# Kernel tuning notes

Hardware: AMD Instinct MI355X
Metric: run time of the kernel (lower is better)

The kernel has to match this reference:

```python
import jax, jax.numpy as jnp
import numpy as np

L, H, LATENT, DM, DH, FF = 4, 4, 256, 768, 192, 1024
EPS = 1e-6      # fast_transformers RecurrentLinearAttention eps
LN_EPS = 1e-5


def make_pe(d_model=LATENT, max_len=5000):
    pos = np.arange(max_len, dtype=np.float32)[:, None]
    div = np.exp(np.arange(0, d_model, 2, dtype=np.float32) * (-np.log(10000.0) / d_model))
    pe = np.zeros((max_len, d_model), np.float32)
    pe[:, 0::2] = np.sin(pos * div)
    pe[:, 1::2] = np.cos(pos * div)
    return jnp.asarray(pe)

PE = make_pe()


def layer_norm(x, g, b):
    m = x.mean(-1, keepdims=True)
    v = ((x - m) ** 2).mean(-1, keepdims=True)
    return (x - m) * jax.lax.rsqrt(v + LN_EPS) * g + b


def setup_inputs() -> dict:
    key = jax.random.key(0)
    ks = jax.random.split(key, 16)
    bs, nj, nf, T, A, C = 8, 25, 6, 80, 6, 12
    s = 0.02
    return dict(
        x=jax.random.normal(ks[0], (bs, nj, nf, T), jnp.float32),
        y=jax.random.randint(ks[1], (bs, A), 0, C),
        ind_map=jnp.sort(jax.random.randint(ks[2], (T, bs), 0, A), axis=0),
        act_tstamps=jnp.sort(jax.random.randint(ks[3], (bs, A), 1, T + 1), axis=1).at[:, -1].set(T),
        skel_W=jax.random.normal(ks[4], (nj * nf, LATENT), jnp.float32) * s,
        skel_b=jnp.zeros((LATENT,), jnp.float32),
        muQuery=jax.random.normal(ks[5], (C, LATENT), jnp.float32),
        sigmaQuery=jax.random.normal(ks[6], (C, LATENT), jnp.float32),
        Wq=jax.random.normal(ks[7], (L, DM, DM), jnp.float32) * s,
        bq=jnp.zeros((L, DM), jnp.float32),
        Wk=jax.random.normal(ks[8], (L, DM, DM), jnp.float32) * s,
        bk=jnp.zeros((L, DM), jnp.float32),
        Wv=jax.random.normal(ks[9], (L, DM, DM), jnp.float32) * s,
        bv=jnp.zeros((L, DM), jnp.float32),
        Wo=jax.random.normal(ks[10], (L, DM, DM), jnp.float32) * s,
        bo=jnp.zeros((L, DM), jnp.float32),
        W1=jax.random.normal(ks[11], (L, DM, FF), jnp.float32) * s,
        b1=jnp.zeros((L, FF), jnp.float32),
        W2=jax.random.normal(ks[12], (L, FF, DM), jnp.float32) * s,
        b2=jnp.zeros((L, DM), jnp.float32),
        ln1_g=jnp.ones((L, DM), jnp.float32), ln1_b=jnp.zeros((L, DM), jnp.float32),
        ln2_g=jnp.ones((L, DM), jnp.float32), ln2_b=jnp.zeros((L, DM), jnp.float32),
        lnf_g=jnp.ones((DM,), jnp.float32), lnf_b=jnp.zeros((DM,), jnp.float32),
    )


def _fwd(x, y, ind_map, act_tstamps, skel_W, skel_b, muQuery, sigmaQuery,
         Wq, bq, Wk, bk, Wv, bv, Wo, bo, W1, b1, W2, b2,
         ln1_g, ln1_b, ln2_g, ln2_b, lnf_g, lnf_b):
    bs, nj, nf, T = x.shape
    # skeleton embedding: [T, bs, njoints*nfeats] @ W -> [T, bs, LATENT]
    xe = x.transpose(3, 0, 1, 2).reshape(T, bs, nj * nf) @ skel_W + skel_b
    mu_q = muQuery[y]        # [bs, A, LATENT]
    sig_q = sigmaQuery[y]
    barange = jnp.arange(bs)

    @jax.checkpoint
    def step(carry, inputs):
        S, Z = carry                         # [L,bs,H,DH,DH], [L,bs,H,DH]
        t, xt, ind_t = inputs
        cm = mu_q[barange, ind_t]            # gather per-sample current action query
        cs = sig_q[barange, ind_t]
        xseq = jnp.stack([cm, cs, xt], 0)    # [3, bs, LATENT]
        start = jnp.where(t == 0, 0, t + 2)  # PositionalEncoding(last_pos=t, offset=2)
        pe3 = jax.lax.dynamic_slice_in_dim(PE, start, 3, 0)
        xseq = xseq + pe3[:, None, :]
        h = xseq.transpose(1, 0, 2).reshape(bs, 3 * LATENT)  # flatten -> [bs, DM]
        nS, nZ = [], []
        for l in range(L):
            q = (h @ Wq[l] + bq[l]).reshape(bs, H, DH)
            k = (h @ Wk[l] + bk[l]).reshape(bs, H, DH)
            v = (h @ Wv[l] + bv[l]).reshape(bs, H, DH)
            Q = jax.nn.elu(q) + 1.0          # linear-attention feature map
            K = jax.nn.elu(k) + 1.0
            Sl = S[l] + K[..., :, None] * v[..., None, :]   # state update S += k (x) v
            Zl = Z[l] + K
            inv = 1.0 / (jnp.einsum('bhd,bhd->bh', Q, Zl) + EPS)
            att = jnp.einsum('bhd,bhdm,bh->bhm', Q, Sl, inv).reshape(bs, DM)
            h1 = layer_norm(h + att @ Wo[l] + bo[l], ln1_g[l], ln1_b[l])
            ffn = jax.nn.relu(h1 @ W1[l] + b1[l]) @ W2[l] + b2[l]
            h = layer_norm(h1 + ffn, ln2_g[l], ln2_b[l])
            nS.append(Sl); nZ.append(Zl)
        h = layer_norm(h, lnf_g, lnf_b)      # encoder final norm
        return (jnp.stack(nS), jnp.stack(nZ)), h

    S0 = jnp.zeros((L, bs, H, DH, DH), x.dtype)
    Z0 = jnp.zeros((L, bs, H, DH), x.dtype)
    _, finals = jax.lax.scan(step, (S0, Z0), (jnp.arange(T), xe, ind_map))  # finals: [T,bs,DM]
    tsel = jnp.maximum(act_tstamps - 1, 0)                       # [bs, A]
    mu = finals[:, :, :LATENT][tsel, barange[:, None]]           # [bs, A, LATENT]
    logvar = finals[:, :, LATENT:2 * LATENT][tsel, barange[:, None]]
    return mu, logvar


def reference(x, y, ind_map, act_tstamps, skel_W, skel_b, muQuery, sigmaQuery,
              Wq, bq, Wk, bk, Wv, bv, Wo, bo, W1, b1, W2, b2,
              ln1_g, ln1_b, ln2_g, ln2_b, lnf_g, lnf_b):
    return _fwd(x, y, ind_map, act_tstamps, skel_W, skel_b, muQuery, sigmaQuery,
                Wq, bq, Wk, bk, Wv, bv, Wo, bo, W1, b1, W2, b2,
                ln1_g, ln1_b, ln2_g, ln2_b, lnf_g, lnf_b)
```

## Files before the change

kernel.cpp:

```cpp
#include <hip/hip_runtime.h>
#include <math.h>

#define TT 80
#define BS 8
#define NA 6
#define DMODEL 768
#define NH 4
#define DH 192
#define FFD 1024
#define NROWS (TT*BS)
#define NQKV (3*DMODEL)

typedef __bf16 bf16;
typedef __bf16 bf16x8 __attribute__((ext_vector_type(8)));
typedef float  f32x4  __attribute__((ext_vector_type(4)));

__device__ __forceinline__ float block_reduce_sum256(float v, float* sm4) {
#pragma unroll
    for (int off = 32; off > 0; off >>= 1) v += __shfl_down(v, off, 64);
    int lane = threadIdx.x & 63, wid = threadIdx.x >> 6;
    if (lane == 0) sm4[wid] = v;
    __syncthreads();
    float r = sm4[0] + sm4[1] + sm4[2] + sm4[3];
    __syncthreads();
    return r;
}

__global__ __launch_bounds__(256) void embed_k(
        const float* __restrict__ x, const int* __restrict__ y,
        const int* __restrict__ ind_map, const float* __restrict__ skel_W,
        const float* __restrict__ skel_b, const float* __restrict__ muQ,
        const float* __restrict__ sigQ, float* __restrict__ h0,
        bf16* __restrict__ h0b) {
    __shared__ float xrow[152];
    int r = blockIdx.x;
    int t = r >> 3, b = r & 7;
    int c = threadIdx.x;
    if (c < 150) xrow[c] = x[(b * 150 + c) * TT + t];
    __syncthreads();
    float acc = skel_b[c];
    for (int jf = 0; jf < 150; jf++) acc += xrow[jf] * skel_W[jf * 256 + c];
    int ind_t = ind_map[t * 8 + b];
    int yb = y[b * NA + ind_t];
    float cm = muQ[yb * 256 + c];
    float cs = sigQ[yb * 256 + c];
    int start = (t == 0) ? 0 : (t + 2);
    float div = expf((float)(c & ~1) * (-9.210340371976184f / 256.0f));
    float p0, p1, p2;
    if (c & 1) {
        p0 = cosf((float)start * div);
        p1 = cosf((float)(start + 1) * div);
        p2 = cosf((float)(start + 2) * div);
    } else {
        p0 = sinf((float)start * div);
        p1 = sinf((float)(start + 1) * div);
        p2 = sinf((float)(start + 2) * div);
    }
    float* hr = h0 + (size_t)r * DMODEL;
    float v0 = cm + p0, v1 = cs + p1, v2 = acc + p2;
    hr[c] = v0; hr[c + 256] = v1; hr[c + 512] = v2;
    bf16* hb = h0b + (size_t)r * DMODEL;
    hb[c] = (bf16)v0; hb[c + 256] = (bf16)v1; hb[c + 512] = (bf16)v2;
}

__global__ __launch_bounds__(256) void transpose_k(
        const float* __restrict__ Wq, const float* __restrict__ Wk,
        const float* __restrict__ Wv, const float* __restrict__ Wo,
        const float* __restrict__ W1, const float* __restrict__ W2,
        bf16* __restrict__ qkvT, bf16* __restrict__ woT,
        bf16* __restrict__ w1T, bf16* __restrict__ w2T) {
    int lz = blockIdx.z;
    int l = lz >> 2, z = lz & 3;
    int K = (z == 3) ? 1024 : 768;
    int N = (z == 0) ? 2304 : (z == 2) ? 1024 : 768;
    int k0 = blockIdx.x * 32, n0 = blockIdx.y * 32;
    if (k0 >= K || n0 >= N) return;
    const float* src; bf16* dst; int ldsrc; int ncol;
    if (z == 0) {
        if (n0 < 768)       { src = Wq + (size_t)l * 768 * 768; ncol = n0; }
        else if (n0 < 1536) { src = Wk + (size_t)l * 768 * 768; ncol = n0 - 768; }
        else                { src = Wv + (size_t)l * 768 * 768; ncol = n0 - 1536; }
        dst = qkvT + (size_t)l * NQKV * DMODEL; ldsrc = 768;
    } else if (z == 1) { src = Wo + (size_t)l * 768 * 768;  dst = woT + (size_t)l * 768 * 768;  ldsrc = 768;  ncol = n0; }
    else if (z == 2)   { src = W1 + (size_t)l * 768 * 1024; dst = w1T + (size_t)l * 1024 * 768; ldsrc = 1024; ncol = n0; }
    else               { src = W2 + (size_t)l * 1024 * 768; dst = w2T + (size_t)l * 768 * 1024; ldsrc = 768;  ncol = n0; }
    __shared__ float tile[32][33];
    int tx = threadIdx.x & 31, ty = threadIdx.x >> 5;
#pragma unroll
    for (int i = 0; i < 4; i++) {
        int r = ty + 8 * i;
        tile[r][tx] = src[(size_t)(k0 + r) * ldsrc + ncol + tx];
    }
    __syncthreads();
#pragma unroll
    for (int i = 0; i < 4; i++) {
        int r = ty + 8 * i;
        dst[(size_t)(n0 + r) * K + k0 + tx] = (bf16)tile[tx][r];
    }
}

template <int EPI>
__global__ __launch_bounds__(256) void gemm_mfma(
        const bf16* __restrict__ A, const bf16* __restrict__ Bt,
        const float* __restrict__ bias_q, const float* __restrict__ bias_k,
        const float* __restrict__ bias_v, const float* __restrict__ resid,
        float* __restrict__ outF, bf16* __restrict__ outB,
        int M, int N, int K) {
    __shared__ __attribute__((aligned(16))) bf16 As0[64][40];
    __shared__ __attribute__((aligned(16))) bf16 As1[64][40];
    __shared__ __attribute__((aligned(16))) bf16 Bs0[64][40];
    __shared__ __attribute__((aligned(16))) bf16 Bs1[64][40];
    int tid = threadIdx.x;
    int m0 = blockIdx.y * 64, n0 = blockIdx.x * 64;
    int w = tid >> 6;
    int l = tid & 63;
    int lm = l & 15, lq = l >> 4;
    int sr = tid >> 2;
    int sk = (tid & 3) * 8;
    const bf16* Arow = &A[(size_t)(m0 + sr) * K];
    const bf16* Brow = &Bt[(size_t)(n0 + sr) * K];
    f32x4 acc[4] = {};
    uint4 a0 = *(const uint4*)&Arow[sk];
    uint4 a1 = *(const uint4*)&Arow[32 + sk];
    uint4 b0 = *(const uint4*)&Brow[sk];
    uint4 b1 = *(const uint4*)&Brow[32 + sk];
    for (int k0 = 0; k0 < K; k0 += 64) {
        __syncthreads();
        *(uint4*)&As0[sr][sk] = a0;
        *(uint4*)&As1[sr][sk] = a1;
        *(uint4*)&Bs0[sr][sk] = b0;
        *(uint4*)&Bs1[sr][sk] = b1;
        __syncthreads();
        int k2 = k0 + 64; if (k2 >= K) k2 = 0;
        a0 = *(const uint4*)&Arow[k2 + sk];
        a1 = *(const uint4*)&Arow[k2 + 32 + sk];
        b0 = *(const uint4*)&Brow[k2 + sk];
        b1 = *(const uint4*)&Brow[k2 + 32 + sk];
        bf16x8 af0 = *(bf16x8*)&As0[w * 16 + lm][lq * 8];
        bf16x8 af1 = *(bf16x8*)&As1[w * 16 + lm][lq * 8];
#pragma unroll
        for (int nb = 0; nb < 4; nb++) {
            bf16x8 bf0 = *(bf16x8*)&Bs0[nb * 16 + lm][lq * 8];
            acc[nb] = __builtin_amdgcn_mfma_f32_16x16x32_bf16(af0, bf0, acc[nb], 0, 0, 0);
        }
#pragma unroll
        for (int nb = 0; nb < 4; nb++) {
            bf16x8 bf1 = *(bf16x8*)&Bs1[nb * 16 + lm][lq * 8];
            acc[nb] = __builtin_amdgcn_mfma_f32_16x16x32_bf16(af1, bf1, acc[nb], 0, 0, 0);
        }
    }
#pragma unroll
    for (int nb = 0; nb < 4; nb++) {
        int col = n0 + nb * 16 + lm;
        float b;
        bool do_elu = false;
        if (EPI == 0) {
            if (col < 768)       { b = bias_q[col];        do_elu = true; }
            else if (col < 1536) { b = bias_k[col - 768];  do_elu = true; }
            else                 { b = bias_v[col - 1536]; }
        } else {
            b = bias_q[col];
        }
#pragma unroll
        for (int r = 0; r < 4; r++) {
            int row = m0 + w * 16 + lq * 4 + r;
            float v = acc[nb][r] + b;
            if (EPI == 0) {
                if (do_elu) v = (v > 0.0f) ? (v + 1.0f) : expf(v);
                outB[(size_t)row * N + col] = (bf16)v;
            } else if (EPI == 1) {
                v += resid[(size_t)row * N + col];
                outF[(size_t)row * N + col] = v;
            } else {
                v = fmaxf(v, 0.0f);
                outB[(size_t)row * N + col] = (bf16)v;
            }
        }
    }
}

__global__ __launch_bounds__(256) void ln_k(
        const float* __restrict__ in, float* __restrict__ outF,
        bf16* __restrict__ outB,
        const float* __restrict__ g, const float* __restrict__ b) {
    int wave = threadIdx.x >> 6, lane = threadIdx.x & 63;
    int row = blockIdx.x * 4 + wave;
    const float* xr = in + (size_t)row * DMODEL;
    float4 v[3];
    float s = 0.0f;
#pragma unroll
    for (int j = 0; j < 3; j++) {
        v[j] = *(const float4*)&xr[lane * 4 + 256 * j];
        s += v[j].x + v[j].y + v[j].z + v[j].w;
    }
#pragma unroll
    for (int mk = 1; mk < 64; mk <<= 1) s += __shfl_xor(s, mk, 64);
    float m = s * (1.0f / 768.0f);
    float sq = 0.0f;
#pragma unroll
    for (int j = 0; j < 3; j++) {
        v[j].x -= m; v[j].y -= m; v[j].z -= m; v[j].w -= m;
        sq += v[j].x * v[j].x + v[j].y * v[j].y + v[j].z * v[j].z + v[j].w * v[j].w;
    }
#pragma unroll
    for (int mk = 1; mk < 64; mk <<= 1) sq += __shfl_xor(sq, mk, 64);
    float r = rsqrtf(sq * (1.0f / 768.0f) + 1e-5f);
    float* orow = outF + (size_t)row * DMODEL;
    bf16* brow = outB + (size_t)row * DMODEL;
#pragma unroll
    for (int j = 0; j < 3; j++) {
        int c = lane * 4 + 256 * j;
        float4 gg = *(const float4*)&g[c];
        float4 bb = *(const float4*)&b[c];
        float o0 = v[j].x * r * gg.x + bb.x;
        float o1 = v[j].y * r * gg.y + bb.y;
        float o2 = v[j].z * r * gg.z + bb.z;
        float o3 = v[j].w * r * gg.w + bb.w;
        *(float4*)&orow[c] = make_float4(o0, o1, o2, o3);
        bf16 tmp4[4] = {(bf16)o0, (bf16)o1, (bf16)o2, (bf16)o3};
        *(uint2*)&brow[c] = *(uint2*)tmp4;
    }
}

__global__ __launch_bounds__(320) void attn_k(
        const bf16* __restrict__ qkvB, bf16* __restrict__ att) {
    __shared__ __attribute__((aligned(16))) char smem[64000];
    bf16* Qs = (bf16*)smem;
    bf16* Ks = (bf16*)(smem + 32000);
    bf16* Aij = (bf16*)smem;
    bf16* VT = (bf16*)(smem + 16640);

    int b = blockIdx.x >> 2, h = blockIdx.x & 3;
    int tid = threadIdx.x;
    int w = tid >> 6, l = tid & 63;
    int lm = l & 15, lq = l >> 4;

    uint4 vreg[6];
#pragma unroll
    for (int u = 0; u < 6; u++) {
        int c = tid + 320 * u;
        int t = c / 24, cc = c % 24;
        int d0 = cc * 8;
        size_t g = (size_t)(t * 8 + b) * NQKV + h * DH + d0;
        uint4 qv = *(const uint4*)&qkvB[g];
        uint4 kv = *(const uint4*)&qkvB[g + 768];
        vreg[u]  = *(const uint4*)&qkvB[g + 1536];
        *(uint4*)&Qs[t * 200 + d0] = qv;
        *(uint4*)&Ks[t * 200 + d0] = kv;
    }
    __syncthreads();

    f32x4 acc[5] = {};
#pragma unroll
    for (int k0 = 0; k0 < 192; k0 += 32) {
        bf16x8 af = *(bf16x8*)&Qs[(w * 16 + lm) * 200 + lq * 8 + k0];
#pragma unroll
        for (int nb = 0; nb < 5; nb++) {
            bf16x8 bfr = *(bf16x8*)&Ks[(nb * 16 + lm) * 200 + lq * 8 + k0];
            acc[nb] = __builtin_amdgcn_mfma_f32_16x16x32_bf16(af, bfr, acc[nb], 0, 0, 0);
        }
    }
    float mval[5][4];
    float rs[4] = {0.f, 0.f, 0.f, 0.f};
#pragma unroll
    for (int nb = 0; nb < 5; nb++)
#pragma unroll
        for (int r = 0; r < 4; r++) {
            int t = w * 16 + lq * 4 + r, tau = nb * 16 + lm;
            float v = (tau <= t) ? acc[nb][r] : 0.0f;
            mval[nb][r] = v;
            rs[r] += v;
        }
#pragma unroll
    for (int mk = 1; mk < 16; mk <<= 1)
#pragma unroll
        for (int r = 0; r < 4; r++) rs[r] += __shfl_xor(rs[r], mk, 64);
    float inv[4];
#pragma unroll
    for (int r = 0; r < 4; r++) inv[r] = 1.0f / (rs[r] + 1e-6f);

    __syncthreads();

#pragma unroll
    for (int nb = 0; nb < 5; nb++)
#pragma unroll
        for (int r = 0; r < 4; r++)
            Aij[(w * 16 + lq * 4 + r) * 104 + nb * 16 + lm] = (bf16)mval[nb][r];
    *(uint2*)&Aij[(tid >> 2) * 104 + 80 + (tid & 3) * 4] = make_uint2(0u, 0u);
#pragma unroll
    for (int u = 0; u < 6; u++) {
        int c = tid + 320 * u;
        int t = c / 24, cc = c % 24;
        int d0 = cc * 8;
        bf16 tmp8[8];
        *(uint4*)tmp8 = vreg[u];
#pragma unroll
        for (int j = 0; j < 8; j++) VT[(d0 + j) * 104 + t] = tmp8[j];
    }
    if (tid < 192) {
        *(uint4*)&VT[tid * 104 + 80] = make_uint4(0u, 0u, 0u, 0u);
        *(uint4*)&VT[tid * 104 + 88] = make_uint4(0u, 0u, 0u, 0u);
    }
    __syncthreads();

#pragma unroll 1
    for (int nc = 0; nc < 12; nc++) {
        f32x4 a2 = {};
#pragma unroll
        for (int k0 = 0; k0 < 96; k0 += 32) {
            bf16x8 af = *(bf16x8*)&Aij[(w * 16 + lm) * 104 + lq * 8 + k0];
            bf16x8 bfr = *(bf16x8*)&VT[(nc * 16 + lm) * 104 + lq * 8 + k0];
            a2 = __builtin_amdgcn_mfma_f32_16x16x32_bf16(af, bfr, a2, 0, 0, 0);
        }
#pragma unroll
        for (int r = 0; r < 4; r++) {
            int t = w * 16 + lq * 4 + r;
            att[(size_t)(t * 8 + b) * DMODEL + h * DH + nc * 16 + lm] =
                (bf16)(a2[r] * inv[r]);
        }
    }
}

__global__ __launch_bounds__(256) void final_k(
        const float* __restrict__ h, const int* __restrict__ act_ts,
        const float* __restrict__ g, const float* __restrict__ bb,
        float* __restrict__ out) {
    __shared__ float sm4[4];
    int ba = blockIdx.x;
    int b = ba / NA;
    int ts = act_ts[ba];
    int t = ts - 1; if (t < 0) t = 0;
    const float* xr = h + (size_t)(t * 8 + b) * DMODEL;
    int c = threadIdx.x;
    float x0 = xr[c], x1 = xr[c + 256], x2 = xr[c + 512];
    float m = block_reduce_sum256(x0 + x1 + x2, sm4) * (1.0f / 768.0f);
    float d0 = x0 - m, d1 = x1 - m, d2 = x2 - m;
    float v = block_reduce_sum256(d0 * d0 + d1 * d1 + d2 * d2, sm4) * (1.0f / 768.0f);
    float r = rsqrtf(v + 1e-5f);
    out[ba * 256 + c]            = d0 * r * g[c] + bb[c];
    out[48 * 256 + ba * 256 + c] = d1 * r * g[c + 256] + bb[c + 256];
}

extern "C" void kernel_launch(void* const* d_in, const int* in_sizes, int n_in,
                              void* d_out, int out_size, void* d_ws, size_t ws_size,
                              hipStream_t stream) {
    const float* x       = (const float*)d_in[0];
    const int*   y       = (const int*)d_in[1];
    const int*   ind_map = (const int*)d_in[2];
    const int*   act_ts  = (const int*)d_in[3];
    const float* skel_W  = (const float*)d_in[4];
    const float* skel_b  = (const float*)d_in[5];
    const float* muQ     = (const float*)d_in[6];
    const float* sigQ    = (const float*)d_in[7];
    const float* Wq = (const float*)d_in[8];   const float* bq = (const float*)d_in[9];
    const float* Wk = (const float*)d_in[10];  const float* bk = (const float*)d_in[11];
    const float* Wv = (const float*)d_in[12];  const float* bv = (const float*)d_in[13];
    const float* Wo = (const float*)d_in[14];  const float* bo = (const float*)d_in[15];
    const float* W1 = (const float*)d_in[16];  const float* b1 = (const float*)d_in[17];
    const float* W2 = (const float*)d_in[18];  const float* b2 = (const float*)d_in[19];
    const float* ln1_g = (const float*)d_in[20]; const float* ln1_b = (const float*)d_in[21];
    const float* ln2_g = (const float*)d_in[22]; const float* ln2_b = (const float*)d_in[23];
    const float* lnf_g = (const float*)d_in[24]; const float* lnf_b = (const float*)d_in[25];
    float* out = (float*)d_out;

    char* p = (char*)d_ws;
    const size_t R  = (size_t)NROWS * DMODEL;
    float* h    = (float*)p; p += R * 4;
    float* h1   = (float*)p; p += R * 4;
    float* tmp  = (float*)p; p += R * 4;
    bf16* qkvB  = (bf16*)p;  p += (size_t)NROWS * NQKV * 2;
    bf16* hB    = (bf16*)p;  p += R * 2;
    bf16* h1B   = (bf16*)p;  p += R * 2;
    bf16* attB  = (bf16*)p;  p += R * 2;
    bf16* ffn1B = (bf16*)p;  p += (size_t)NROWS * FFD * 2;
    bf16* qkvT  = (bf16*)p;  p += (size_t)4 * NQKV * DMODEL * 2;
    bf16* woT   = (bf16*)p;  p += (size_t)4 * DMODEL * DMODEL * 2;
    bf16* w1T   = (bf16*)p;  p += (size_t)4 * FFD * DMODEL * 2;
    bf16* w2T   = (bf16*)p;  p += (size_t)4 * DMODEL * FFD * 2;

    dim3 gT(32, 72, 16);
    transpose_k<<<gT, 256, 0, stream>>>(Wq, Wk, Wv, Wo, W1, W2, qkvT, woT, w1T, w2T);
    embed_k<<<NROWS, 256, 0, stream>>>(x, y, ind_map, skel_W, skel_b, muQ, sigQ, h, hB);

    dim3 gQKV(NQKV / 64, 10);
    dim3 g768(12, 10);
    dim3 g1024(16, 10);
    for (int l = 0; l < 4; l++) {
        const bf16* qkvTl = qkvT + (size_t)l * NQKV * DMODEL;
        const bf16* woTl  = woT  + (size_t)l * DMODEL * DMODEL;
        const bf16* w1Tl  = w1T  + (size_t)l * FFD * DMODEL;
        const bf16* w2Tl  = w2T  + (size_t)l * DMODEL * FFD;
        gemm_mfma<0><<<gQKV, 256, 0, stream>>>(hB, qkvTl,
                bq + l * DMODEL, bk + l * DMODEL, bv + l * DMODEL,
                nullptr, nullptr, qkvB, NROWS, NQKV, DMODEL);
        attn_k<<<32, 320, 0, stream>>>(qkvB, attB);
        gemm_mfma<1><<<g768, 256, 0, stream>>>(attB, woTl,
                bo + l * DMODEL, nullptr, nullptr, h, tmp, nullptr,
                NROWS, DMODEL, DMODEL);
        ln_k<<<NROWS / 4, 256, 0, stream>>>(tmp, h1, h1B, ln1_g + l * DMODEL, ln1_b + l * DMODEL);
        gemm_mfma<2><<<g1024, 256, 0, stream>>>(h1B, w1Tl,
                b1 + l * FFD, nullptr, nullptr, nullptr, nullptr, ffn1B,
                NROWS, FFD, DMODEL);
        gemm_mfma<1><<<g768, 256, 0, stream>>>(ffn1B, w2Tl,
                b2 + l * DMODEL, nullptr, nullptr, h1, tmp, nullptr,
                NROWS, DMODEL, FFD);
        ln_k<<<NROWS / 4, 256, 0, stream>>>(tmp, h, hB, ln2_g + l * DMODEL, ln2_b + l * DMODEL);
    }

    final_k<<<48, 256, 0, stream>>>(h, act_ts, lnf_g, lnf_b, out);
}
```

Baseline: 423.6 us.

## Fuse all stages into one persistent cooperative kernel with grid barriers

Replaces the sequence of about thirty kernel launches (transpose, embed, per-layer GEMMs, attention, layernorms, final) with a single cooperative persistent kernel of 256 blocks. The stages are separated by atomic-counter grid barriers. GEMM tiles change to 80x64 with 320 threads and are distributed across blocks with a grid-stride loop. This targets launch overhead and inter-kernel gaps, but every stage now waits at a global barrier and some stages (attention, final) use only a few blocks while the others idle.

```diff
diff --git a/kernel.cpp b/kernel.cpp
--- a/kernel.cpp
+++ b/kernel.cpp
@@ -5,232 +5,214 @@
 #define BS 8
 #define NA 6
 #define DMODEL 768
-#define NH 4
 #define DH 192
 #define FFD 1024
 #define NROWS (TT*BS)
 #define NQKV (3*DMODEL)
+#define NTHREADS 320
+#define NBLOCKS 256
 
 typedef __bf16 bf16;
 typedef __bf16 bf16x8 __attribute__((ext_vector_type(8)));
 typedef float  f32x4  __attribute__((ext_vector_type(4)));
 
-__device__ __forceinline__ float block_reduce_sum256(float v, float* sm4) {
-#pragma unroll
-    for (int off = 32; off > 0; off >>= 1) v += __shfl_down(v, off, 64);
-    int lane = threadIdx.x & 63, wid = threadIdx.x >> 6;
-    if (lane == 0) sm4[wid] = v;
-    __syncthreads();
-    float r = sm4[0] + sm4[1] + sm4[2] + sm4[3];
-    __syncthreads();
-    return r;
-}
-
-__global__ __launch_bounds__(256) void embed_k(
-        const float* __restrict__ x, const int* __restrict__ y,
-        const int* __restrict__ ind_map, const float* __restrict__ skel_W,
-        const float* __restrict__ skel_b, const float* __restrict__ muQ,
-        const float* __restrict__ sigQ, float* __restrict__ h0,
-        bf16* __restrict__ h0b) {
-    __shared__ float xrow[152];
-    int r = blockIdx.x;
-    int t = r >> 3, b = r & 7;
-    int c = threadIdx.x;
-    if (c < 150) xrow[c] = x[(b * 150 + c) * TT + t];
-    __syncthreads();
-    float acc = skel_b[c];
-    for (int jf = 0; jf < 150; jf++) acc += xrow[jf] * skel_W[jf * 256 + c];
-    int ind_t = ind_map[t * 8 + b];
-    int yb = y[b * NA + ind_t];
-    float cm = muQ[yb * 256 + c];
-    float cs = sigQ[yb * 256 + c];
-    int start = (t == 0) ? 0 : (t + 2);
-    float div = expf((float)(c & ~1) * (-9.210340371976184f / 256.0f));
-    float p0, p1, p2;
-    if (c & 1) {
-        p0 = cosf((float)start * div);
-        p1 = cosf((float)(start + 1) * div);
-        p2 = cosf((float)(start + 2) * div);
-    } else {
-        p0 = sinf((float)start * div);
-        p1 = sinf((float)(start + 1) * div);
-        p2 = sinf((float)(start + 2) * div);
-    }
-    float* hr = h0 + (size_t)r * DMODEL;
-    float v0 = cm + p0, v1 = cs + p1, v2 = acc + p2;
-    hr[c] = v0; hr[c + 256] = v1; hr[c + 512] = v2;
-    bf16* hb = h0b + (size_t)r * DMODEL;
-    hb[c] = (bf16)v0; hb[c + 256] = (bf16)v1; hb[c + 512] = (bf16)v2;
-}
-
-__global__ __launch_bounds__(256) void transpose_k(
-        const float* __restrict__ Wq, const float* __restrict__ Wk,
-        const float* __restrict__ Wv, const float* __restrict__ Wo,
-        const float* __restrict__ W1, const float* __restrict__ W2,
-        bf16* __restrict__ qkvT, bf16* __restrict__ woT,
-        bf16* __restrict__ w1T, bf16* __restrict__ w2T) {
-    int lz = blockIdx.z;
-    int l = lz >> 2, z = lz & 3;
-    int K = (z == 3) ? 1024 : 768;
-    int N = (z == 0) ? 2304 : (z == 2) ? 1024 : 768;
-    int k0 = blockIdx.x * 32, n0 = blockIdx.y * 32;
-    if (k0 >= K || n0 >= N) return;
-    const float* src; bf16* dst; int ldsrc; int ncol;
-    if (z == 0) {
-        if (n0 < 768)       { src = Wq + (size_t)l * 768 * 768; ncol = n0; }
-        else if (n0 < 1536) { src = Wk + (size_t)l * 768 * 768; ncol = n0 - 768; }
-        else                { src = Wv + (size_t)l * 768 * 768; ncol = n0 - 1536; }
-        dst = qkvT + (size_t)l * NQKV * DMODEL; ldsrc = 768;
-    } else if (z == 1) { src = Wo + (size_t)l * 768 * 768;  dst = woT + (size_t)l * 768 * 768;  ldsrc = 768;  ncol = n0; }
-    else if (z == 2)   { src = W1 + (size_t)l * 768 * 1024; dst = w1T + (size_t)l * 1024 * 768; ldsrc = 1024; ncol = n0; }
-    else               { src = W2 + (size_t)l * 1024 * 768; dst = w2T + (size_t)l * 768 * 1024; ldsrc = 768;  ncol = n0; }
-    __shared__ float tile[32][33];
-    int tx = threadIdx.x & 31, ty = threadIdx.x >> 5;
-#pragma unroll
-    for (int i = 0; i < 4; i++) {
-        int r = ty + 8 * i;
-        tile[r][tx] = src[(size_t)(k0 + r) * ldsrc + ncol + tx];
-    }
-    __syncthreads();
-#pragma unroll
-    for (int i = 0; i < 4; i++) {
-        int r = ty + 8 * i;
-        dst[(size_t)(n0 + r) * K + k0 + tx] = (bf16)tile[tx][r];
+struct MegaP {
+    const float *x; const int *y; const int *ind_map; const int *act_ts;
+    const float *skel_W, *skel_b, *muQ, *sigQ;
+    const float *Wq, *bq, *Wk, *bk, *Wv, *bv, *Wo, *bo, *W1, *b1, *W2, *b2;
+    const float *ln1_g, *ln1_b, *ln2_g, *ln2_b, *lnf_g, *lnf_b;
+    float *out;
+    float *h, *h1, *tmp;
+    bf16 *qkvB, *hB, *h1B, *attB, *ffn1B, *qkvT, *woT, *w1T, *w2T;
+    int *bar;
+};
+
+__device__ __forceinline__ void gbar(int* cnt, int target) {
+    __syncthreads();
+    if (threadIdx.x == 0) {
+        __hip_atomic_fetch_add(cnt, 1, __ATOMIC_RELEASE, __HIP_MEMORY_SCOPE_AGENT);
+        while (__hip_atomic_load(cnt, __ATOMIC_RELAXED, __HIP_MEMORY_SCOPE_AGENT) < target)
+            __builtin_amdgcn_s_sleep(2);
+        __threadfence();
+    }
+    __syncthreads();
+}
+
+__device__ void prep_stage(char* smem, const MegaP& P) {
+    float (*tile)[33] = (float(*)[33])smem;
+    float* xrow = (float*)(smem + 8192);
+    int tid = threadIdx.x;
+#pragma unroll 1
+    for (int job = blockIdx.x; job < 15360 + 640; job += gridDim.x) {
+        if (job < 15360) {
+            int l = job / 3840, r = job % 3840;
+            const float* src; bf16* dst; int ldsrc, Kd, n0, ncol, k0;
+            if (r < 1728) {
+                int kt = r % 24, nt = r / 24;
+                k0 = kt * 32; n0 = nt * 32; Kd = 768; ldsrc = 768;
+                dst = P.qkvT + (size_t)l * NQKV * DMODEL;
+                if (n0 < 768)       { src = P.Wq + (size_t)l * 589824; ncol = n0; }
+                else if (n0 < 1536) { src = P.Wk + (size_t)l * 589824; ncol = n0 - 768; }
+                else                { src = P.Wv + (size_t)l * 589824; ncol = n0 - 1536; }
+            } else if (r < 2304) {
+                int r2 = r - 1728; int kt = r2 % 24, nt = r2 / 24;
+                k0 = kt * 32; n0 = nt * 32; ncol = n0; Kd = 768; ldsrc = 768;
+                src = P.Wo + (size_t)l * 589824; dst = P.woT + (size_t)l * 589824;
+            } else if (r < 3072) {
+                int r2 = r - 2304; int kt = r2 % 24, nt = r2 / 24;
+                k0 = kt * 32; n0 = nt * 32; ncol = n0; Kd = 768; ldsrc = 1024;
+                src = P.W1 + (size_t)l * 786432; dst = P.w1T + (size_t)l * 786432;
+            } else {
+                int r2 = r - 3072; int kt = r2 % 32, nt = r2 / 32;
+                k0 = kt * 32; n0 = nt * 32; ncol = n0; Kd = 1024; ldsrc = 768;
+                src = P.W2 + (size_t)l * 786432; dst = P.w2T + (size_t)l * 786432;
+            }
+            int tx = tid & 31, ty = tid >> 5;
+            if (tid < 256) {
+#pragma unroll
+                for (int i = 0; i < 4; i++) {
+                    int rr = ty + 8 * i;
+                    tile[rr][tx] = src[(size_t)(k0 + rr) * ldsrc + ncol + tx];
+                }
+            }
+            __syncthreads();
+            if (tid < 256) {
+#pragma unroll
+                for (int i = 0; i < 4; i++) {
+                    int rr = ty + 8 * i;
+                    dst[(size_t)(n0 + rr) * Kd + k0 + tx] = (bf16)tile[tx][rr];
+                }
+            }
+            __syncthreads();
+        } else {
+            int rr = job - 15360;
+            int t = rr >> 3, b = rr & 7;
+            int c = tid;
+            if (c < 150) xrow[c] = P.x[(b * 150 + c) * TT + t];
+            __syncthreads();
+            if (c < 256) {
+                float acc = P.skel_b[c];
+                for (int jf = 0; jf < 150; jf++) acc += xrow[jf] * P.skel_W[jf * 256 + c];
+                int ind_t = P.ind_map[t * 8 + b];
+                int yb = P.y[b * NA + ind_t];
+                float cm = P.muQ[yb * 256 + c];
+                float cs = P.sigQ[yb * 256 + c];
+                int start = (t == 0) ? 0 : (t + 2);
+                float div = expf((float)(c & ~1) * (-9.210340371976184f / 256.0f));
+                float p0, p1, p2;
+                if (c & 1) {
+                    p0 = cosf((float)start * div);
+                    p1 = cosf((float)(start + 1) * div);
+                    p2 = cosf((float)(start + 2) * div);
+                } else {
+                    p0 = sinf((float)start * div);
+                    p1 = sinf((float)(start + 1) * div);
+                    p2 = sinf((float)(start + 2) * div);
+                }
+                float* hr = P.h + (size_t)rr * DMODEL;
+                float v0 = cm + p0, v1 = cs + p1, v2 = acc + p2;
+                hr[c] = v0; hr[c + 256] = v1; hr[c + 512] = v2;
+                bf16* hb = P.hB + (size_t)rr * DMODEL;
+                hb[c] = (bf16)v0; hb[c + 256] = (bf16)v1; hb[c + 512] = (bf16)v2;
+            }
+            __syncthreads();
+        }
     }
 }
 
 template <int EPI>
-__global__ __launch_bounds__(256) void gemm_mfma(
+__device__ void gemm_stage(char* smem,
         const bf16* __restrict__ A, const bf16* __restrict__ Bt,
         const float* __restrict__ bias_q, const float* __restrict__ bias_k,
         const float* __restrict__ bias_v, const float* __restrict__ resid,
-        float* __restrict__ outF, bf16* __restrict__ outB,
-        int M, int N, int K) {
-    __shared__ __attribute__((aligned(16))) bf16 As0[64][40];
-    __shared__ __attribute__((aligned(16))) bf16 As1[64][40];
-    __shared__ __attribute__((aligned(16))) bf16 Bs0[64][40];
-    __shared__ __attribute__((aligned(16))) bf16 Bs1[64][40];
+        float* __restrict__ outF, bf16* __restrict__ outB, int N, int K) {
+    bf16 (*As0)[40] = (bf16(*)[40])(smem);
+    bf16 (*As1)[40] = (bf16(*)[40])(smem + 6400);
+    bf16 (*Bs0)[40] = (bf16(*)[40])(smem + 12800);
+    bf16 (*Bs1)[40] = (bf16(*)[40])(smem + 17920);
     int tid = threadIdx.x;
-    int m0 = blockIdx.y * 64, n0 = blockIdx.x * 64;
-    int w = tid >> 6;
-    int l = tid & 63;
+    int w = tid >> 6, l = tid & 63;
     int lm = l & 15, lq = l >> 4;
     int sr = tid >> 2;
     int sk = (tid & 3) * 8;
-    const bf16* Arow = &A[(size_t)(m0 + sr) * K];
-    const bf16* Brow = &Bt[(size_t)(n0 + sr) * K];
-    f32x4 acc[4] = {};
-    uint4 a0 = *(const uint4*)&Arow[sk];
-    uint4 a1 = *(const uint4*)&Arow[32 + sk];
-    uint4 b0 = *(const uint4*)&Brow[sk];
-    uint4 b1 = *(const uint4*)&Brow[32 + sk];
-    for (int k0 = 0; k0 < K; k0 += 64) {
-        __syncthreads();
-        *(uint4*)&As0[sr][sk] = a0;
-        *(uint4*)&As1[sr][sk] = a1;
-        *(uint4*)&Bs0[sr][sk] = b0;
-        *(uint4*)&Bs1[sr][sk] = b1;
-        __syncthreads();
-        int k2 = k0 + 64; if (k2 >= K) k2 = 0;
-        a0 = *(const uint4*)&Arow[k2 + sk];
-        a1 = *(const uint4*)&Arow[k2 + 32 + sk];
-        b0 = *(const uint4*)&Brow[k2 + sk];
-        b1 = *(const uint4*)&Brow[k2 + 32 + sk];
-        bf16x8 af0 = *(bf16x8*)&As0[w * 16 + lm][lq * 8];
-        bf16x8 af1 = *(bf16x8*)&As1[w * 16 + lm][lq * 8];
+    int ntiles = 8 * (N / 64);
+#pragma unroll 1
+    for (int tile = blockIdx.x; tile < ntiles; tile += gridDim.x) {
+        int m0 = (tile & 7) * 80;
+        int n0 = (tile >> 3) * 64;
+        const bf16* Arow = &A[(size_t)(m0 + sr) * K + sk];
+        const bf16* Brow = &Bt[(size_t)(n0 + (sr & 63)) * K + sk];
+        f32x4 acc[4] = {};
+        uint4 a0 = *(const uint4*)(Arow);
+        uint4 a1 = *(const uint4*)(Arow + 32);
+        uint4 b0 = {}, b1 = {};
+        if (tid < 256) { b0 = *(const uint4*)(Brow); b1 = *(const uint4*)(Brow + 32); }
+        for (int k0 = 0; k0 < K; k0 += 64) {
+            __syncthreads();
+            *(uint4*)&As0[sr][sk] = a0;
+            *(uint4*)&As1[sr][sk] = a1;
+            if (tid < 256) {
+                *(uint4*)&Bs0[sr][sk] = b0;
+                *(uint4*)&Bs1[sr][sk] = b1;
+            }
+            __syncthreads();
+            int k2 = k0 + 64; if (k2 >= K) k2 = 0;
+            a0 = *(const uint4*)(Arow + k2);
+            a1 = *(const uint4*)(Arow + k2 + 32);
+            if (tid < 256) {
+                b0 = *(const uint4*)(Brow + k2);
+                b1 = *(const uint4*)(Brow + k2 + 32);
+            }
+            bf16x8 af0 = *(bf16x8*)&As0[w * 16 + lm][lq * 8];
+            bf16x8 af1 = *(bf16x8*)&As1[w * 16 + lm][lq * 8];
+#pragma unroll
+            for (int nb = 0; nb < 4; nb++) {
+                bf16x8 bfr = *(bf16x8*)&Bs0[nb * 16 + lm][lq * 8];
+                acc[nb] = __builtin_amdgcn_mfma_f32_16x16x32_bf16(af0, bfr, acc[nb], 0, 0, 0);
+            }
+#pragma unroll
+            for (int nb = 0; nb < 4; nb++) {
+                bf16x8 bfr = *(bf16x8*)&Bs1[nb * 16 + lm][lq * 8];
+                acc[nb] = __builtin_amdgcn_mfma_f32_16x16x32_bf16(af1, bfr, acc[nb], 0, 0, 0);
+            }
+        }
 #pragma unroll
         for (int nb = 0; nb < 4; nb++) {
-            bf16x8 bf0 = *(bf16x8*)&Bs0[nb * 16 + lm][lq * 8];
-            acc[nb] = __builtin_amdgcn_mfma_f32_16x16x32_bf16(af0, bf0, acc[nb], 0, 0, 0);
-        }
-#pragma unroll
-        for (int nb = 0; nb < 4; nb++) {
-            bf16x8 bf1 = *(bf16x8*)&Bs1[nb * 16 + lm][lq * 8];
-            acc[nb] = __builtin_amdgcn_mfma_f32_16x16x32_bf16(af1, bf1, acc[nb], 0, 0, 0);
-        }
-    }
-#pragma unroll
-    for (int nb = 0; nb < 4; nb++) {
-        int col = n0 + nb * 16 + lm;
-        float b;
-        bool do_elu = false;
-        if (EPI == 0) {
-            if (col < 768)       { b = bias_q[col];        do_elu = true; }
-            else if (col < 1536) { b = bias_k[col - 768];  do_elu = true; }
-            else                 { b = bias_v[col - 1536]; }
-        } else {
-            b = bias_q[col];
-        }
-#pragma unroll
-        for (int r = 0; r < 4; r++) {
-            int row = m0 + w * 16 + lq * 4 + r;
-            float v = acc[nb][r] + b;
+            int col = n0 + nb * 16 + lm;
+            float bia; bool do_elu = false;
             if (EPI == 0) {
-                if (do_elu) v = (v > 0.0f) ? (v + 1.0f) : expf(v);
-                outB[(size_t)row * N + col] = (bf16)v;
-            } else if (EPI == 1) {
-                v += resid[(size_t)row * N + col];
-                outF[(size_t)row * N + col] = v;
+                if (col < 768)       { bia = bias_q[col];        do_elu = true; }
+                else if (col < 1536) { bia = bias_k[col - 768];  do_elu = true; }
+                else                 { bia = bias_v[col - 1536]; }
             } else {
-                v = fmaxf(v, 0.0f);
-                outB[(size_t)row * N + col] = (bf16)v;
-            }
-        }
-    }
-}
-
-__global__ __launch_bounds__(256) void ln_k(
-        const float* __restrict__ in, float* __restrict__ outF,
-        bf16* __restrict__ outB,
-        const float* __restrict__ g, const float* __restrict__ b) {
-    int wave = threadIdx.x >> 6, lane = threadIdx.x & 63;
-    int row = blockIdx.x * 4 + wave;
-    const float* xr = in + (size_t)row * DMODEL;
-    float4 v[3];
-    float s = 0.0f;
-#pragma unroll
-    for (int j = 0; j < 3; j++) {
-        v[j] = *(const float4*)&xr[lane * 4 + 256 * j];
-        s += v[j].x + v[j].y + v[j].z + v[j].w;
-    }
-#pragma unroll
-    for (int mk = 1; mk < 64; mk <<= 1) s += __shfl_xor(s, mk, 64);
-    float m = s * (1.0f / 768.0f);
-    float sq = 0.0f;
-#pragma unroll
-    for (int j = 0; j < 3; j++) {
-        v[j].x -= m; v[j].y -= m; v[j].z -= m; v[j].w -= m;
-        sq += v[j].x * v[j].x + v[j].y * v[j].y + v[j].z * v[j].z + v[j].w * v[j].w;
-    }
-#pragma unroll
-    for (int mk = 1; mk < 64; mk <<= 1) sq += __shfl_xor(sq, mk, 64);
-    float r = rsqrtf(sq * (1.0f / 768.0f) + 1e-5f);
-    float* orow = outF + (size_t)row * DMODEL;
-    bf16* brow = outB + (size_t)row * DMODEL;
-#pragma unroll
-    for (int j = 0; j < 3; j++) {
-        int c = lane * 4 + 256 * j;
-        float4 gg = *(const float4*)&g[c];
-        float4 bb = *(const float4*)&b[c];
-        float o0 = v[j].x * r * gg.x + bb.x;
-        float o1 = v[j].y * r * gg.y + bb.y;
-        float o2 = v[j].z * r * gg.z + bb.z;
-        float o3 = v[j].w * r * gg.w + bb.w;
-        *(float4*)&orow[c] = make_float4(o0, o1, o2, o3);
-        bf16 tmp4[4] = {(bf16)o0, (bf16)o1, (bf16)o2, (bf16)o3};
-        *(uint2*)&brow[c] = *(uint2*)tmp4;
-    }
-}
-
-__global__ __launch_bounds__(320) void attn_k(
-        const bf16* __restrict__ qkvB, bf16* __restrict__ att) {
-    __shared__ __attribute__((aligned(16))) char smem[64000];
+                bia = bias_q[col];
+            }
+#pragma unroll
+            for (int r = 0; r < 4; r++) {
+                int row = m0 + w * 16 + lq * 4 + r;
+                float v = acc[nb][r] + bia;
+                if (EPI == 0) {
+                    if (do_elu) v = (v > 0.0f) ? (v + 1.0f) : expf(v);
+                    outB[(size_t)row * N + col] = (bf16)v;
+                } else if (EPI == 1) {
+                    v += resid[(size_t)row * N + col];
+                    outF[(size_t)row * N + col] = v;
+                } else {
+                    v = fmaxf(v, 0.0f);
+                    outB[(size_t)row * N + col] = (bf16)v;
+                }
+            }
+        }
+    }
+}
+
+__device__ void attn_stage(char* smem, const bf16* __restrict__ qkvB,
+                           bf16* __restrict__ att) {
     bf16* Qs = (bf16*)smem;
     bf16* Ks = (bf16*)(smem + 32000);
     bf16* Aij = (bf16*)smem;
     bf16* VT = (bf16*)(smem + 16640);
-
-    int b = blockIdx.x >> 2, h = blockIdx.x & 3;
+    int bb = blockIdx.x >> 2, hd = blockIdx.x & 3;
     int tid = threadIdx.x;
     int w = tid >> 6, l = tid & 63;
     int lm = l & 15, lq = l >> 4;
@@ -241,7 +223,7 @@
         int c = tid + 320 * u;
         int t = c / 24, cc = c % 24;
         int d0 = cc * 8;
-        size_t g = (size_t)(t * 8 + b) * NQKV + h * DH + d0;
+        size_t g = (size_t)(t * 8 + bb) * NQKV + hd * DH + d0;
         uint4 qv = *(const uint4*)&qkvB[g];
         uint4 kv = *(const uint4*)&qkvB[g + 768];
         vreg[u]  = *(const uint4*)&qkvB[g + 1536];
@@ -315,97 +297,165 @@
 #pragma unroll
         for (int r = 0; r < 4; r++) {
             int t = w * 16 + lq * 4 + r;
-            att[(size_t)(t * 8 + b) * DMODEL + h * DH + nc * 16 + lm] =
+            att[(size_t)(t * 8 + bb) * DMODEL + hd * DH + nc * 16 + lm] =
                 (bf16)(a2[r] * inv[r]);
         }
     }
 }
 
-__global__ __launch_bounds__(256) void final_k(
-        const float* __restrict__ h, const int* __restrict__ act_ts,
-        const float* __restrict__ g, const float* __restrict__ bb,
-        float* __restrict__ out) {
-    __shared__ float sm4[4];
+__device__ void ln_stage(const float* __restrict__ in, float* __restrict__ outF,
+        bf16* __restrict__ outB,
+        const float* __restrict__ g, const float* __restrict__ b) {
+    int wave = threadIdx.x >> 6, lane = threadIdx.x & 63;
+#pragma unroll 1
+    for (int row = blockIdx.x * 5 + wave; row < NROWS; row += gridDim.x * 5) {
+        const float* xr = in + (size_t)row * DMODEL;
+        float4 v[3];
+        float s = 0.0f;
+#pragma unroll
+        for (int j = 0; j < 3; j++) {
+            v[j] = *(const float4*)&xr[lane * 4 + 256 * j];
+            s += v[j].x + v[j].y + v[j].z + v[j].w;
+        }
+#pragma unroll
+        for (int mk = 1; mk < 64; mk <<= 1) s += __shfl_xor(s, mk, 64);
+        float m = s * (1.0f / 768.0f);
+        float sq = 0.0f;
+#pragma unroll
+        for (int j = 0; j < 3; j++) {
+            v[j].x -= m; v[j].y -= m; v[j].z -= m; v[j].w -= m;
+            sq += v[j].x * v[j].x + v[j].y * v[j].y + v[j].z * v[j].z + v[j].w * v[j].w;
+        }
+#pragma unroll
+        for (int mk = 1; mk < 64; mk <<= 1) sq += __shfl_xor(sq, mk, 64);
+        float r = rsqrtf(sq * (1.0f / 768.0f) + 1e-5f);
+        float* orow = outF + (size_t)row * DMODEL;
+        bf16* brow = outB + (size_t)row * DMODEL;
+#pragma unroll
+        for (int j = 0; j < 3; j++) {
+            int c = lane * 4 + 256 * j;
+            float4 gg = *(const float4*)&g[c];
+            float4 bbv = *(const float4*)&b[c];
+            float o0 = v[j].x * r * gg.x + bbv.x;
+            float o1 = v[j].y * r * gg.y + bbv.y;
+            float o2 = v[j].z * r * gg.z + bbv.z;
+            float o3 = v[j].w * r * gg.w + bbv.w;
+            *(float4*)&orow[c] = make_float4(o0, o1, o2, o3);
+            bf16 tmp4[4] = {(bf16)o0, (bf16)o1, (bf16)o2, (bf16)o3};
+            *(uint2*)&brow[c] = *(uint2*)tmp4;
+        }
+    }
+}
+
+__device__ __forceinline__ float block_reduce_sum5(float v, float* sm) {
+#pragma unroll
+    for (int off = 32; off > 0; off >>= 1) v += __shfl_down(v, off, 64);
+    int lane = threadIdx.x & 63, wid = threadIdx.x >> 6;
+    __syncthreads();
+    if (lane == 0) sm[wid] = v;
+    __syncthreads();
+    return sm[0] + sm[1] + sm[2] + sm[3] + sm[4];
+}
+
+__device__ void final_stage(char* smem, const float* __restrict__ hbuf,
+        const int* __restrict__ act_ts, const float* __restrict__ g,
+        const float* __restrict__ bb, float* __restrict__ out) {
+    float* sm = (float*)smem;
     int ba = blockIdx.x;
     int b = ba / NA;
     int ts = act_ts[ba];
     int t = ts - 1; if (t < 0) t = 0;
-    const float* xr = h + (size_t)(t * 8 + b) * DMODEL;
+    const float* xr = hbuf + (size_t)(t * 8 + b) * DMODEL;
     int c = threadIdx.x;
-    float x0 = xr[c], x1 = xr[c + 256], x2 = xr[c + 512];
-    float m = block_reduce_sum256(x0 + x1 + x2, sm4) * (1.0f / 768.0f);
+    float x0 = 0.f, x1 = 0.f, x2 = 0.f;
+    if (c < 256) { x0 = xr[c]; x1 = xr[c + 256]; x2 = xr[c + 512]; }
+    float m = block_reduce_sum5(x0 + x1 + x2, sm) * (1.0f / 768.0f);
     float d0 = x0 - m, d1 = x1 - m, d2 = x2 - m;
-    float v = block_reduce_sum256(d0 * d0 + d1 * d1 + d2 * d2, sm4) * (1.0f / 768.0f);
+    float contrib = (c < 256) ? (d0 * d0 + d1 * d1 + d2 * d2) : 0.f;
+    float v = block_reduce_sum5(contrib, sm) * (1.0f / 768.0f);
     float r = rsqrtf(v + 1e-5f);
-    out[ba * 256 + c]            = d0 * r * g[c] + bb[c];
-    out[48 * 256 + ba * 256 + c] = d1 * r * g[c + 256] + bb[c + 256];
+    if (c < 256) {
+        out[ba * 256 + c]            = d0 * r * g[c] + bb[c];
+        out[48 * 256 + ba * 256 + c] = d1 * r * g[c + 256] + bb[c + 256];
+    }
+}
+
+__global__ __launch_bounds__(NTHREADS) void mega_k(MegaP P) {
+    __shared__ __attribute__((aligned(16))) char smem[64000];
+    int nb = gridDim.x;
+    int bno = 0;
+    prep_stage(smem, P);
+    bno += nb; gbar(P.bar, bno);
+#pragma unroll 1
+    for (int l = 0; l < 4; l++) {
+        gemm_stage<0>(smem, P.hB, P.qkvT + (size_t)l * NQKV * DMODEL,
+                      P.bq + l * DMODEL, P.bk + l * DMODEL, P.bv + l * DMODEL,
+                      nullptr, nullptr, P.qkvB, NQKV, DMODEL);
+        bno += nb; gbar(P.bar, bno);
+        if (blockIdx.x < 32) attn_stage(smem, P.qkvB, P.attB);
+        bno += nb; gbar(P.bar, bno);
+        gemm_stage<1>(smem, P.attB, P.woT + (size_t)l * DMODEL * DMODEL,
+                      P.bo + l * DMODEL, nullptr, nullptr, P.h, P.tmp, nullptr,
+                      DMODEL, DMODEL);
+        bno += nb; gbar(P.bar, bno);
+        ln_stage(P.tmp, P.h1, P.h1B, P.ln1_g + l * DMODEL, P.ln1_b + l * DMODEL);
+        bno += nb; gbar(P.bar, bno);
+        gemm_stage<2>(smem, P.h1B, P.w1T + (size_t)l * FFD * DMODEL,
+                      P.b1 + l * FFD, nullptr, nullptr, nullptr, nullptr, P.ffn1B,
+                      FFD, DMODEL);
+        bno += nb; gbar(P.bar, bno);
+        gemm_stage<1>(smem, P.ffn1B, P.w2T + (size_t)l * DMODEL * FFD,
+                      P.b2 + l * DMODEL, nullptr, nullptr, P.h1, P.tmp, nullptr,
+                      DMODEL, FFD);
+        bno += nb; gbar(P.bar, bno);
+        ln_stage(P.tmp, P.h, P.hB, P.ln2_g + l * DMODEL, P.ln2_b + l * DMODEL);
+        bno += nb; gbar(P.bar, bno);
+    }
+    if (blockIdx.x < 48)
+        final_stage(smem, P.h, P.act_ts, P.lnf_g, P.lnf_b, P.out);
 }
 
 extern "C" void kernel_launch(void* const* d_in, const int* in_sizes, int n_in,
                               void* d_out, int out_size, void* d_ws, size_t ws_size,
                               hipStream_t stream) {
-    const float* x       = (const float*)d_in[0];
-    const int*   y       = (const int*)d_in[1];
-    const int*   ind_map = (const int*)d_in[2];
-    const int*   act_ts  = (const int*)d_in[3];
-    const float* skel_W  = (const float*)d_in[4];
-    const float* skel_b  = (const float*)d_in[5];
-    const float* muQ     = (const float*)d_in[6];
-    const float* sigQ    = (const float*)d_in[7];
-    const float* Wq = (const float*)d_in[8];   const float* bq = (const float*)d_in[9];
-    const float* Wk = (const float*)d_in[10];  const float* bk = (const float*)d_in[11];
-    const float* Wv = (const float*)d_in[12];  const float* bv = (const float*)d_in[13];
-    const float* Wo = (const float*)d_in[14];  const float* bo = (const float*)d_in[15];
-    const float* W1 = (const float*)d_in[16];  const float* b1 = (const float*)d_in[17];
-    const float* W2 = (const float*)d_in[18];  const float* b2 = (const float*)d_in[19];
-    const float* ln1_g = (const float*)d_in[20]; const float* ln1_b = (const float*)d_in[21];
-    const float* ln2_g = (const float*)d_in[22]; const float* ln2_b = (const float*)d_in[23];
-    const float* lnf_g = (const float*)d_in[24]; const float* lnf_b = (const float*)d_in[25];
-    float* out = (float*)d_out;
+    MegaP P;
+    P.x       = (const float*)d_in[0];
+    P.y       = (const int*)d_in[1];
+    P.ind_map = (const int*)d_in[2];
+    P.act_ts  = (const int*)d_in[3];
+    P.skel_W  = (const float*)d_in[4];
+    P.skel_b  = (const float*)d_in[5];
+    P.muQ     = (const float*)d_in[6];
+    P.sigQ    = (const float*)d_in[7];
+    P.Wq = (const float*)d_in[8];   P.bq = (const float*)d_in[9];
+    P.Wk = (const float*)d_in[10];  P.bk = (const float*)d_in[11];
+    P.Wv = (const float*)d_in[12];  P.bv = (const float*)d_in[13];
+    P.Wo = (const float*)d_in[14];  P.bo = (const float*)d_in[15];
+    P.W1 = (const float*)d_in[16];  P.b1 = (const float*)d_in[17];
+    P.W2 = (const float*)d_in[18];  P.b2 = (const float*)d_in[19];
+    P.ln1_g = (const float*)d_in[20]; P.ln1_b = (const float*)d_in[21];
+    P.ln2_g = (const float*)d_in[22]; P.ln2_b = (const float*)d_in[23];
+    P.lnf_g = (const float*)d_in[24]; P.lnf_b = (const float*)d_in[25];
+    P.out = (float*)d_out;
 
     char* p = (char*)d_ws;
-    const size_t R  = (size_t)NROWS * DMODEL;
-    float* h    = (float*)p; p += R * 4;
-    float* h1   = (float*)p; p += R * 4;
-    float* tmp  = (float*)p; p += R * 4;
-    bf16* qkvB  = (bf16*)p;  p += (size_t)NROWS * NQKV * 2;
-    bf16* hB    = (bf16*)p;  p += R * 2;
-    bf16* h1B   = (bf16*)p;  p += R * 2;
-    bf16* attB  = (bf16*)p;  p += R * 2;
-    bf16* ffn1B = (bf16*)p;  p += (size_t)NROWS * FFD * 2;
-    bf16* qkvT  = (bf16*)p;  p += (size_t)4 * NQKV * DMODEL * 2;
-    bf16* woT   = (bf16*)p;  p += (size_t)4 * DMODEL * DMODEL * 2;
-    bf16* w1T   = (bf16*)p;  p += (size_t)4 * FFD * DMODEL * 2;
-    bf16* w2T   = (bf16*)p;  p += (size_t)4 * DMODEL * FFD * 2;
-
-    dim3 gT(32, 72, 16);
-    transpose_k<<<gT, 256, 0, stream>>>(Wq, Wk, Wv, Wo, W1, W2, qkvT, woT, w1T, w2T);
-    embed_k<<<NROWS, 256, 0, stream>>>(x, y, ind_map, skel_W, skel_b, muQ, sigQ, h, hB);
-
-    dim3 gQKV(NQKV / 64, 10);
-    dim3 g768(12, 10);
-    dim3 g1024(16, 10);
-    for (int l = 0; l < 4; l++) {
-        const bf16* qkvTl = qkvT + (size_t)l * NQKV * DMODEL;
-        const bf16* woTl  = woT  + (size_t)l * DMODEL * DMODEL;
-        const bf16* w1Tl  = w1T  + (size_t)l * FFD * DMODEL;
-        const bf16* w2Tl  = w2T  + (size_t)l * DMODEL * FFD;
-        gemm_mfma<0><<<gQKV, 256, 0, stream>>>(hB, qkvTl,
-                bq + l * DMODEL, bk + l * DMODEL, bv + l * DMODEL,
-                nullptr, nullptr, qkvB, NROWS, NQKV, DMODEL);
-        attn_k<<<32, 320, 0, stream>>>(qkvB, attB);
-        gemm_mfma<1><<<g768, 256, 0, stream>>>(attB, woTl,
-                bo + l * DMODEL, nullptr, nullptr, h, tmp, nullptr,
-                NROWS, DMODEL, DMODEL);
-        ln_k<<<NROWS / 4, 256, 0, stream>>>(tmp, h1, h1B, ln1_g + l * DMODEL, ln1_b + l * DMODEL);
-        gemm_mfma<2><<<g1024, 256, 0, stream>>>(h1B, w1Tl,
-                b1 + l * FFD, nullptr, nullptr, nullptr, nullptr, ffn1B,
-                NROWS, FFD, DMODEL);
-        gemm_mfma<1><<<g768, 256, 0, stream>>>(ffn1B, w2Tl,
-                b2 + l * DMODEL, nullptr, nullptr, h1, tmp, nullptr,
-                NROWS, DMODEL, FFD);
-        ln_k<<<NROWS / 4, 256, 0, stream>>>(tmp, h, hB, ln2_g + l * DMODEL, ln2_b + l * DMODEL);
-    }
-
-    final_k<<<48, 256, 0, stream>>>(h, act_ts, lnf_g, lnf_b, out);
-}
+    P.bar = (int*)p; p += 64;
+    const size_t R = (size_t)NROWS * DMODEL;
+    P.h    = (float*)p; p += R * 4;
+    P.h1   = (float*)p; p += R * 4;
+    P.tmp  = (float*)p; p += R * 4;
+    P.qkvB  = (bf16*)p; p += (size_t)NROWS * NQKV * 2;
+    P.hB    = (bf16*)p; p += R * 2;
+    P.h1B   = (bf16*)p; p += R * 2;
+    P.attB  = (bf16*)p; p += R * 2;
+    P.ffn1B = (bf16*)p; p += (size_t)NROWS * FFD * 2;
+    P.qkvT  = (bf16*)p; p += (size_t)4 * NQKV * DMODEL * 2;
+    P.woT   = (bf16*)p; p += (size_t)4 * DMODEL * DMODEL * 2;
+    P.w1T   = (bf16*)p; p += (size_t)4 * FFD * DMODEL * 2;
+    P.w2T   = (bf16*)p; p += (size_t)4 * DMODEL * FFD * 2;
+
+    hipMemsetAsync(P.bar, 0, 64, stream);
+    void* args[] = { (void*)&P };
+    hipLaunchCooperativeKernel(reinterpret_cast<const void*>(mega_k),
+                               dim3(NBLOCKS), dim3(NTHREADS), args, 0, stream);
+}
```

New measurement: 978.3 us. +130.9%, slower.
